# Kernel optimization log

Hardware: AMD Instinct MI355X
Metric: run time of the kernel (lower is better)

The kernel has to match this reference:

```python
import jax, jax.numpy as jnp
import numpy as np

B, S, H, NH, HD, F, L = 512, 32, 1024, 16, 64, 2048, 6
OBS_D, REF_D, ACT_D, MAX_REL = 256, 128, 32, 32
SCALE = 1.0 / np.sqrt(HD)
LN_EPS = 1e-5


def _ln(x, g, b):
    mu = x.mean(-1, keepdims=True)
    var = ((x - mu) ** 2).mean(-1, keepdims=True)
    return (x - mu) * jax.lax.rsqrt(var + LN_EPS) * g + b


def _mlp3(x, w0, b0, w1, b1, w2, b2):
    h = jax.nn.relu(x @ w0 + b0)
    h = jax.nn.relu(h @ w1 + b1)
    return h @ w2 + b2


def setup_inputs() -> dict:
    key = jax.random.key(0)
    ks = iter(jax.random.split(key, 64))

    def n(shape, scale=1.0):
        return (jax.random.normal(next(ks), shape, dtype=jnp.float32) * scale)

    W = 0.02  # weight scale (xavier-ish) to keep activations sane
    inp = {
        'obs': n((B, S, OBS_D)), 'ref': n((B, S, REF_D)),
        'obs_w0': n((OBS_D, 512), W), 'obs_b0': jnp.zeros((512,), jnp.float32),
        'obs_w1': n((512, 256), W), 'obs_b1': jnp.zeros((256,), jnp.float32),
        'obs_w2': n((256, H), W), 'obs_b2': jnp.zeros((H,), jnp.float32),
        'ref_w0': n((REF_D, 256), W), 'ref_b0': jnp.zeros((256,), jnp.float32),
        'ref_w1': n((256, 256), W), 'ref_b1': jnp.zeros((256,), jnp.float32),
        'ref_w2': n((256, H), W), 'ref_b2': jnp.zeros((H,), jnp.float32),
        'pos_emb': n((64, H), W),
        'Wq': n((L, H, H), W), 'Wk': n((L, H, H), W), 'Wv': n((L, H, H), W),
        'Wo': n((L, H, H), W), 'bo': jnp.zeros((L, H), jnp.float32),
        'rel_emb': n((L, 2 * MAX_REL + 1, HD), W),
        'ff_w1': n((L, H, F), W), 'ff_b1': jnp.zeros((L, F), jnp.float32),
        'ff_w2': n((L, F, H), W), 'ff_b2': jnp.zeros((L, H), jnp.float32),
        'ln1_g': jnp.ones((L, H), jnp.float32), 'ln1_b': jnp.zeros((L, H), jnp.float32),
        'ln2_g': jnp.ones((L, H), jnp.float32), 'ln2_b': jnp.zeros((L, H), jnp.float32),
        'act_w0': n((H, 256), W), 'act_b0': jnp.zeros((256,), jnp.float32),
        'act_w1': n((256, 128), W), 'act_b1': jnp.zeros((128,), jnp.float32),
        'act_w2': n((128, ACT_D), W), 'act_b2': jnp.zeros((ACT_D,), jnp.float32),
    }
    return inp


def _forward(obs, ref, obs_w0, obs_b0, obs_w1, obs_b1, obs_w2, obs_b2,
             ref_w0, ref_b0, ref_w1, ref_b1, ref_w2, ref_b2, pos_emb,
             Wq, Wk, Wv, Wo, bo, rel_emb, ff_w1, ff_b1, ff_w2, ff_b2,
             ln1_g, ln1_b, ln2_g, ln2_b,
             act_w0, act_b0, act_w1, act_b1, act_w2, act_b2):
    b, s, _ = obs.shape
    x = _mlp3(obs, obs_w0, obs_b0, obs_w1, obs_b1, obs_w2, obs_b2)
    x = x + _mlp3(ref, ref_w0, ref_b0, ref_w1, ref_b1, ref_w2, ref_b2)
    x = x + pos_emb[:s][None]  # learned positional encoding

    idx = jnp.arange(s)
    rel_idx = jnp.clip(idx[:, None] - idx[None, :], -MAX_REL, MAX_REL) + MAX_REL  # [S,S]

    def block(h, p):
        wq, wk, wv, wo, b_o, rel, w1, b1, w2, b2, g1, be1, g2, be2 = p
        xn = _ln(h, g1, be1)
        q = (xn @ wq).reshape(b, s, NH, HD)
        k = (xn @ wk).reshape(b, s, NH, HD)
        v = (xn @ wv).reshape(b, s, NH, HD)
        scores = jnp.einsum('bqhd,bkhd->bhqk', q, k) * SCALE
        rel_e = rel[rel_idx]  # [S,S,HD]
        scores = scores + jnp.einsum('bqhd,qkd->bhqk', q, rel_e)
        attn = jax.nn.softmax(scores, axis=-1)
        o = jnp.einsum('bhqk,bkhd->bqhd', attn, v).reshape(b, s, H)
        h = h + o @ wo + b_o
        xn2 = _ln(h, g2, be2)
        ff = jax.nn.gelu(xn2 @ w1 + b1, approximate=False) @ w2 + b2
        return h + ff, None

    x, _ = jax.lax.scan(block, x, (Wq, Wk, Wv, Wo, bo, rel_emb,
                                    ff_w1, ff_b1, ff_w2, ff_b2,
                                    ln1_g, ln1_b, ln2_g, ln2_b))
    return _mlp3(x[:, -1], act_w0, act_b0, act_w1, act_b1, act_w2, act_b2)


def reference(obs, ref, obs_w0, obs_b0, obs_w1, obs_b1, obs_w2, obs_b2,
              ref_w0, ref_b0, ref_w1, ref_b1, ref_w2, ref_b2, pos_emb,
              Wq, Wk, Wv, Wo, bo, rel_emb, ff_w1, ff_b1, ff_w2, ff_b2,
              ln1_g, ln1_b, ln2_g, ln2_b,
              act_w0, act_b0, act_w1, act_b1, act_w2, act_b2):
    return _forward(obs, ref, obs_w0, obs_b0, obs_w1, obs_b1, obs_w2, obs_b2,
                    ref_w0, ref_b0, ref_w1, ref_b1, ref_w2, ref_b2, pos_emb,
                    Wq, Wk, Wv, Wo, bo, rel_emb, ff_w1, ff_b1, ff_w2, ff_b2,
                    ln1_g, ln1_b, ln2_g, ln2_b,
                    act_w0, act_b0, act_w1, act_b1, act_w2, act_b2)
```

## Files before the change

### kernel.cpp

```cpp
#include <hip/hip_runtime.h>
#include <cstdint>
#include <cstddef>

typedef unsigned short u16;
typedef float f32x4 __attribute__((ext_vector_type(4)));
typedef short s16x8 __attribute__((ext_vector_type(8)));
typedef __bf16 bf16x8 __attribute__((ext_vector_type(8)));

#define DEVINL __device__ __forceinline__

DEVINL float bf2f(u16 u){ union{unsigned int i; float f;} c; c.i=((unsigned int)u)<<16; return c.f; }
DEVINL u16 f2bf(float f){ union{float f; unsigned int i;} c; c.f=f; unsigned int u=c.i;
                          u += 0x7FFF + ((u>>16)&1); return (u16)(u>>16); }

DEVINL f32x4 mfma16(bf16x8 a, bf16x8 b, f32x4 c){
  return __builtin_amdgcn_mfma_f32_16x16x32_bf16(a, b, c, 0, 0, 0);
}

typedef const __attribute__((address_space(1))) void* gas1p;
typedef __attribute__((address_space(3))) void* as3p;
DEVINL void async16(const void* g, void* l){
  __builtin_amdgcn_global_load_lds((gas1p)g, (as3p)l, 16, 0, 0);
}


__global__ void cvt_bf16(const float* __restrict__ in, u16* __restrict__ out, int n){
  int i = (blockIdx.x * 256 + threadIdx.x) * 4;
  if (i >= n) return;
  float4 v = *(const float4*)(in + i);
  short4 sv = make_short4((short)f2bf(v.x), (short)f2bf(v.y), (short)f2bf(v.z), (short)f2bf(v.w));
  *(short4*)(out + i) = sv;
}

__global__ __launch_bounds__(256) void trans_w(const float* __restrict__ W, u16* __restrict__ WT,
                                               int K, int N){
  __shared__ float t[32][33];
  const float* Wm = W  + (size_t)blockIdx.z * K * N;
  u16*         Tm = WT + (size_t)blockIdx.z * K * N;
  const int x = threadIdx.x, y = threadIdx.y;
  const int n0 = blockIdx.x * 32, k0 = blockIdx.y * 32;
#pragma unroll
  for (int j = 0; j < 32; j += 8)
    t[y + j][x] = Wm[(size_t)(k0 + y + j) * N + n0 + x];
  __syncthreads();
#pragma unroll
  for (int j = 0; j < 32; j += 8)
    Tm[(size_t)(n0 + y + j) * K + k0 + x] = f2bf(t[x][y + j]);
}


__global__ __launch_bounds__(256) void gemm128(
    const u16* __restrict__ A, const u16* __restrict__ BT,
    const float* __restrict__ bias, const float* __restrict__ resid,
    const float* __restrict__ pos, void* __restrict__ out,
    int M, int N, int K, int fuse)
{
  __shared__ u16 As[2][4096];
  __shared__ u16 Bs[2][4096];
  const int tid = threadIdx.x;
  const int bn = blockIdx.x, bm = blockIdx.y;
  const int lane = tid & 63, wid = tid >> 6;
  const int lr = lane & 15, lk = lane >> 4;
  const int wm = (wid >> 1) * 64, wn = (wid & 1) * 64;

  f32x4 acc[4][4] = {};

  const int r0 = tid >> 2;
  const int c0 = (tid & 3) * 8;
  const u16* Ab = A  + (size_t)(bm * 128 + r0) * K + c0;
  const u16* Bb = BT + (size_t)(bn * 128 + r0) * K + c0;
  const size_t rstep = (size_t)64 * K;
  const int nk = K >> 5;

  async16(Ab,         &As[0][tid * 8]);
  async16(Ab + rstep, &As[0][2048 + tid * 8]);
  async16(Bb,         &Bs[0][tid * 8]);
  async16(Bb + rstep, &Bs[0][2048 + tid * 8]);

  int cur = 0;
  for (int kt = 0; kt < nk; ++kt){
    __syncthreads();
    if (kt + 1 < nk){
      const u16* An = Ab + (size_t)(kt + 1) * 32;
      const u16* Bn = Bb + (size_t)(kt + 1) * 32;
      u16* Asn = &As[cur ^ 1][0];
      u16* Bsn = &Bs[cur ^ 1][0];
      async16(An,         Asn + tid * 8);
      async16(An + rstep, Asn + 2048 + tid * 8);
      async16(Bn,         Bsn + tid * 8);
      async16(Bn + rstep, Bsn + 2048 + tid * 8);
    }
    bf16x8 af[4], bfv[4];
#pragma unroll
    for (int i = 0; i < 4; ++i)
      af[i] = *(const bf16x8*)&As[cur][(wm + i * 16 + lr) * 32 + lk * 8];
#pragma unroll
    for (int j = 0; j < 4; ++j)
      bfv[j] = *(const bf16x8*)&Bs[cur][(wn + j * 16 + lr) * 32 + lk * 8];
#pragma unroll
    for (int i = 0; i < 4; ++i)
#pragma unroll
      for (int j = 0; j < 4; ++j)
        acc[i][j] = mfma16(af[i], bfv[j], acc[i][j]);
    cur ^= 1;
  }

  const int gm0 = bm * 128 + wm, gn0 = bn * 128 + wn;
  float* outf = (float*)out;
  u16*   outb = (u16*)out;
#pragma unroll
  for (int i = 0; i < 4; ++i){
#pragma unroll
    for (int j = 0; j < 4; ++j){
      const int col = gn0 + j * 16 + lr;
      const float bv = bias ? bias[col] : 0.f;
#pragma unroll
      for (int r = 0; r < 4; ++r){
        const int row = gm0 + i * 16 + lk * 4 + r;
        const size_t idx = (size_t)row * N + col;
        float v = acc[i][j][r] + bv;
        if (fuse == 1)      v = fmaxf(v, 0.f);
        else if (fuse == 2) v = 0.5f * v * (1.f + erff(v * 0.70710678118654752f));
        else if (fuse == 4) v += resid[idx];
        else if (fuse == 5) v += resid[idx] + pos[((row & 31) << 10) + col];
        if (fuse >= 3) outf[idx] = v;
        else           outb[idx] = f2bf(v);
      }
    }
  }
}


__global__ __launch_bounds__(256) void ln_k(
    const float* __restrict__ x, const float* __restrict__ g,
    const float* __restrict__ b, u16* __restrict__ out)
{
  const int row = blockIdx.x;
  const float* xr = x + (size_t)row * 1024;
  const int tid = threadIdx.x;
  float4 v = *(const float4*)(xr + tid * 4);
  float s  = v.x + v.y + v.z + v.w;
  float ss = v.x * v.x + v.y * v.y + v.z * v.z + v.w * v.w;
#pragma unroll
  for (int m = 1; m < 64; m <<= 1){ s += __shfl_xor(s, m, 64); ss += __shfl_xor(ss, m, 64); }
  __shared__ float red[8];
  if ((tid & 63) == 0){ red[tid >> 6] = s; red[4 + (tid >> 6)] = ss; }
  __syncthreads();
  s  = red[0] + red[1] + red[2] + red[3];
  ss = red[4] + red[5] + red[6] + red[7];
  const float mu = s * (1.f / 1024.f);
  const float rs = rsqrtf(ss * (1.f / 1024.f) - mu * mu + 1e-5f);
  float4 gg = *(const float4*)(g + tid * 4);
  float4 bb = *(const float4*)(b + tid * 4);
  short4 sv = make_short4((short)f2bf((v.x - mu) * rs * gg.x + bb.x),
                          (short)f2bf((v.y - mu) * rs * gg.y + bb.y),
                          (short)f2bf((v.z - mu) * rs * gg.z + bb.z),
                          (short)f2bf((v.w - mu) * rs * gg.w + bb.w));
  *(short4*)(out + (size_t)row * 1024 + tid * 4) = sv;
}


__global__ __launch_bounds__(256) void attn_k(
    const u16* __restrict__ Q, const u16* __restrict__ Kx,
    const u16* __restrict__ V, const u16* __restrict__ rel,
    u16* __restrict__ O)
{
  __shared__ char smem[65536];
  const int tid = threadIdx.x;
  const int wid = tid >> 6, lane = tid & 63;
  const int lr = lane & 15, lk = lane >> 4;
  char* sw = smem + wid * 16384;
  float* P = (float*)sw;
  u16*  AL = (u16*)(sw + 8704);
  u16*  VT = (u16*)(sw + 11264);

  const int pair = blockIdx.x * 4 + wid;
  const int b = pair >> 4, h = pair & 15;
  const size_t base = (size_t)b * 32768 + (size_t)h * 64;
  const u16* q  = Q  + base;
  const u16* kk = Kx + base;
  const u16* v  = V  + base;
  u16* o = O + base;

  s16x8 vv[4];
#pragma unroll
  for (int j = 0; j < 4; ++j){
    const int e = j * 64 + lane;
    const int ki = e >> 3, d0 = (e & 7) * 8;
    vv[j] = *(const s16x8*)(v + (size_t)ki * 1024 + d0);
  }

  bf16x8 qf[2][2], kf[2][2];
#pragma unroll
  for (int mf = 0; mf < 2; ++mf)
#pragma unroll
    for (int ks = 0; ks < 2; ++ks){
      qf[mf][ks] = *(const bf16x8*)(q  + (size_t)(mf * 16 + lr) * 1024 + ks * 32 + lk * 8);
      kf[mf][ks] = *(const bf16x8*)(kk + (size_t)(mf * 16 + lr) * 1024 + ks * 32 + lk * 8);
    }

  f32x4 sc[2][2] = {};
#pragma unroll
  for (int mf = 0; mf < 2; ++mf)
#pragma unroll
    for (int nf = 0; nf < 2; ++nf){
      sc[mf][nf] = mfma16(qf[mf][0], kf[nf][0], sc[mf][nf]);
      sc[mf][nf] = mfma16(qf[mf][1], kf[nf][1], sc[mf][nf]);
      sc[mf][nf] *= 0.125f;
    }

  f32x4 p[2][4] = {};
#pragma unroll
  for (int nf = 0; nf < 4; ++nf){
    bf16x8 rf0 = *(const bf16x8*)(rel + (nf * 16 + lr) * 64 + lk * 8);
    bf16x8 rf1 = *(const bf16x8*)(rel + (nf * 16 + lr) * 64 + 32 + lk * 8);
#pragma unroll
    for (int mf = 0; mf < 2; ++mf){
      p[mf][nf] = mfma16(qf[mf][0], rf0, p[mf][nf]);
      p[mf][nf] = mfma16(qf[mf][1], rf1, p[mf][nf]);
    }
  }

#pragma unroll
  for (int j = 0; j < 4; ++j){
    const int e = j * 64 + lane;
    const int ki = e >> 3, d0 = (e & 7) * 8;
#pragma unroll
    for (int i = 0; i < 8; ++i)
      VT[(d0 + i) * 40 + ki] = (u16)vv[j][i];
  }
#pragma unroll
  for (int mf = 0; mf < 2; ++mf)
#pragma unroll
    for (int nf = 0; nf < 4; ++nf)
#pragma unroll
      for (int r = 0; r < 4; ++r)
        P[(mf * 16 + lk * 4 + r) * 68 + nf * 16 + lr] = p[mf][nf][r];

  __syncthreads();

#pragma unroll
  for (int mf = 0; mf < 2; ++mf)
#pragma unroll
    for (int n2 = 0; n2 < 2; ++n2)
#pragma unroll
      for (int r = 0; r < 4; ++r){
        const int qr = mf * 16 + lk * 4 + r;
        const int kc = n2 * 16 + lr;
        sc[mf][n2][r] += P[qr * 68 + (qr - kc + 32)];
      }

#pragma unroll
  for (int mf = 0; mf < 2; ++mf)
#pragma unroll
    for (int r = 0; r < 4; ++r){
      float mx = fmaxf(sc[mf][0][r], sc[mf][1][r]);
#pragma unroll
      for (int m2 = 1; m2 < 16; m2 <<= 1) mx = fmaxf(mx, __shfl_xor(mx, m2, 64));
      const float e0 = __expf(sc[mf][0][r] - mx);
      const float e1 = __expf(sc[mf][1][r] - mx);
      float sm = e0 + e1;
#pragma unroll
      for (int m2 = 1; m2 < 16; m2 <<= 1) sm += __shfl_xor(sm, m2, 64);
      const float inv = 1.f / sm;
      sc[mf][0][r] = e0 * inv;
      sc[mf][1][r] = e1 * inv;
    }

#pragma unroll
  for (int mf = 0; mf < 2; ++mf)
#pragma unroll
    for (int n2 = 0; n2 < 2; ++n2)
#pragma unroll
      for (int r = 0; r < 4; ++r)
        AL[(mf * 16 + lk * 4 + r) * 40 + n2 * 16 + lr] = f2bf(sc[mf][n2][r]);

  __syncthreads();

  bf16x8 paf[2];
  paf[0] = *(const bf16x8*)&AL[(lr) * 40 + lk * 8];
  paf[1] = *(const bf16x8*)&AL[(16 + lr) * 40 + lk * 8];

  f32x4 of[2][4] = {};
#pragma unroll
  for (int nf = 0; nf < 4; ++nf){
    bf16x8 vf = *(const bf16x8*)&VT[(nf * 16 + lr) * 40 + lk * 8];
    of[0][nf] = mfma16(paf[0], vf, of[0][nf]);
    of[1][nf] = mfma16(paf[1], vf, of[1][nf]);
  }
#pragma unroll
  for (int mf = 0; mf < 2; ++mf)
#pragma unroll
    for (int nf = 0; nf < 4; ++nf)
#pragma unroll
      for (int r = 0; r < 4; ++r)
        o[(size_t)(mf * 16 + lk * 4 + r) * 1024 + nf * 16 + lr] = f2bf(of[mf][nf][r]);
}


__global__ void gather_last(const float* __restrict__ x, u16* __restrict__ out){
  const int i = blockIdx.x * 256 + threadIdx.x;
  const int b = i >> 10, c = i & 1023;
  out[i] = f2bf(x[((size_t)b * 32 + 31) * 1024 + c]);
}

__global__ void small_gemm(const u16* __restrict__ A, const u16* __restrict__ BT,
                           const float* __restrict__ bias, void* __restrict__ out,
                           int M, int N, int K, int fuse){
  const int idx = blockIdx.x * 256 + threadIdx.x;
  if (idx >= M * N) return;
  const int m = idx / N, n = idx - m * N;
  const u16* a  = A  + (size_t)m * K;
  const u16* bt = BT + (size_t)n * K;
  float acc = 0.f;
  for (int k = 0; k < K; k += 8){
    s16x8 av = *(const s16x8*)(a + k);
    s16x8 bv = *(const s16x8*)(bt + k);
#pragma unroll
    for (int i = 0; i < 8; ++i) acc += bf2f((u16)av[i]) * bf2f((u16)bv[i]);
  }
  float v = acc + bias[n];
  if (fuse == 1) v = fmaxf(v, 0.f);
  if (fuse == 3) ((float*)out)[idx] = v;
  else           ((u16*)out)[idx]   = f2bf(v);
}


extern "C" void kernel_launch(void* const* d_in, const int* in_sizes, int n_in,
                              void* d_out, int out_size, void* d_ws, size_t ws_size,
                              hipStream_t stream)
{
  (void)in_sizes; (void)n_in; (void)out_size;
  const float* obs    = (const float*)d_in[0];
  const float* refp   = (const float*)d_in[1];
  const float* obs_w0 = (const float*)d_in[2];
  const float* obs_b0 = (const float*)d_in[3];
  const float* obs_w1 = (const float*)d_in[4];
  const float* obs_b1 = (const float*)d_in[5];
  const float* obs_w2 = (const float*)d_in[6];
  const float* obs_b2 = (const float*)d_in[7];
  const float* ref_w0 = (const float*)d_in[8];
  const float* ref_b0 = (const float*)d_in[9];
  const float* ref_w1 = (const float*)d_in[10];
  const float* ref_b1 = (const float*)d_in[11];
  const float* ref_w2 = (const float*)d_in[12];
  const float* ref_b2 = (const float*)d_in[13];
  const float* pos    = (const float*)d_in[14];
  const float* Wq     = (const float*)d_in[15];
  const float* Wk     = (const float*)d_in[16];
  const float* Wv     = (const float*)d_in[17];
  const float* Wo     = (const float*)d_in[18];
  const float* bo     = (const float*)d_in[19];
  const float* rel    = (const float*)d_in[20];
  const float* ff_w1  = (const float*)d_in[21];
  const float* ff_b1  = (const float*)d_in[22];
  const float* ff_w2  = (const float*)d_in[23];
  const float* ff_b2  = (const float*)d_in[24];
  const float* ln1g   = (const float*)d_in[25];
  const float* ln1b   = (const float*)d_in[26];
  const float* ln2g   = (const float*)d_in[27];
  const float* ln2b   = (const float*)d_in[28];
  const float* act_w0 = (const float*)d_in[29];
  const float* act_b0 = (const float*)d_in[30];
  const float* act_w1 = (const float*)d_in[31];
  const float* act_b1 = (const float*)d_in[32];
  const float* act_w2 = (const float*)d_in[33];
  const float* act_b2 = (const float*)d_in[34];
  float* outp = (float*)d_out;

  char* wsp = (char*)d_ws; size_t off = 0;
  auto alloc = [&](size_t bytes)->char*{ char* p = wsp + off;
                                         off = (off + bytes + 255) & ~(size_t)255; return p; };

  u16* wt_obs0 = (u16*)alloc((size_t)512 * 256 * 2);
  u16* wt_obs1 = (u16*)alloc((size_t)256 * 512 * 2);
  u16* wt_obs2 = (u16*)alloc((size_t)1024 * 256 * 2);
  u16* wt_ref0 = (u16*)alloc((size_t)256 * 128 * 2);
  u16* wt_ref1 = (u16*)alloc((size_t)256 * 256 * 2);
  u16* wt_ref2 = (u16*)alloc((size_t)1024 * 256 * 2);
  u16* wt_a0   = (u16*)alloc((size_t)256 * 1024 * 2);
  u16* wt_a1   = (u16*)alloc((size_t)128 * 256 * 2);
  u16* wt_a2   = (u16*)alloc((size_t)32 * 128 * 2);
  u16* rel_bf  = (u16*)alloc((size_t)6 * 65 * 64 * 2);
  u16* wt_lq   = (u16*)alloc((size_t)1024 * 1024 * 2);
  u16* wt_lk   = (u16*)alloc((size_t)1024 * 1024 * 2);
  u16* wt_lv   = (u16*)alloc((size_t)1024 * 1024 * 2);
  u16* wt_lo   = (u16*)alloc((size_t)1024 * 1024 * 2);
  u16* wt_lf1  = (u16*)alloc((size_t)2048 * 1024 * 2);
  u16* wt_lf2  = (u16*)alloc((size_t)2048 * 1024 * 2);
  float* x     = (float*)alloc((size_t)16384 * 1024 * 4);
  u16* xn      = (u16*)alloc((size_t)16384 * 1024 * 2);
  u16* qb      = (u16*)alloc((size_t)16384 * 1024 * 2);
  u16* kb      = (u16*)alloc((size_t)16384 * 1024 * 2);
  u16* vb      = (u16*)alloc((size_t)16384 * 1024 * 2);

  if (off > ws_size) return;

  u16* obs_bf = qb;
  u16* h1     = kb;
  u16* h2     = vb;
  u16* ref_bf = xn;
  u16* ob     = xn;
  u16* ffb    = qb;
  u16* xlast  = qb;
  u16* a1b    = kb;
  u16* a2b    = vb;

  auto CV = [&](const float* src, u16* dst, int n){
    cvt_bf16<<<dim3((n / 4 + 255) / 256), dim3(256), 0, stream>>>(src, dst, n);
  };
  auto TR = [&](const float* W, u16* WT, int Kd, int Nd, int nz){
    trans_w<<<dim3(Nd / 32, Kd / 32, nz), dim3(32, 8), 0, stream>>>(W, WT, Kd, Nd);
  };
  auto GM = [&](const u16* A, const u16* BT, const float* bias, const float* resid,
                const float* posb, void* op, int Md, int Nd, int Kd, int fuse){
    gemm128<<<dim3(Nd / 128, Md / 128), dim3(256), 0, stream>>>(A, BT, bias, resid, posb, op, Md, Nd, Kd, fuse);
  };

  CV(rel, rel_bf, 6 * 65 * 64);
  TR(obs_w0, wt_obs0, 256, 512, 1);
  TR(obs_w1, wt_obs1, 512, 256, 1);
  TR(obs_w2, wt_obs2, 256, 1024, 1);
  TR(ref_w0, wt_ref0, 128, 256, 1);
  TR(ref_w1, wt_ref1, 256, 256, 1);
  TR(ref_w2, wt_ref2, 256, 1024, 1);
  TR(act_w0, wt_a0, 1024, 256, 1);
  TR(act_w1, wt_a1, 256, 128, 1);
  TR(act_w2, wt_a2, 128, 32, 1);

  const int M = 16384;
  CV(obs, obs_bf, 16384 * 256);
  GM(obs_bf, wt_obs0, obs_b0, nullptr, nullptr, h1, M, 512, 256, 1);
  GM(h1,     wt_obs1, obs_b1, nullptr, nullptr, h2, M, 256, 512, 1);
  GM(h2,     wt_obs2, obs_b2, nullptr, nullptr, x,  M, 1024, 256, 3);
  CV(refp, ref_bf, 16384 * 128);
  GM(ref_bf, wt_ref0, ref_b0, nullptr, nullptr, h2, M, 256, 128, 1);
  GM(h2,     wt_ref1, ref_b1, nullptr, nullptr, h1, M, 256, 256, 1);
  GM(h1,     wt_ref2, ref_b2, x, pos,           x,  M, 1024, 256, 5);

  for (int l = 0; l < 6; ++l){
    TR(Wq + (size_t)l * 1048576, wt_lq, 1024, 1024, 1);
    TR(Wk + (size_t)l * 1048576, wt_lk, 1024, 1024, 1);
    TR(Wv + (size_t)l * 1048576, wt_lv, 1024, 1024, 1);
    TR(Wo + (size_t)l * 1048576, wt_lo, 1024, 1024, 1);
    TR(ff_w1 + (size_t)l * 2097152, wt_lf1, 1024, 2048, 1);
    TR(ff_w2 + (size_t)l * 2097152, wt_lf2, 2048, 1024, 1);

    ln_k<<<dim3(16384), dim3(256), 0, stream>>>(x, ln1g + l * 1024, ln1b + l * 1024, xn);
    GM(xn, wt_lq, nullptr, nullptr, nullptr, qb, M, 1024, 1024, 0);
    GM(xn, wt_lk, nullptr, nullptr, nullptr, kb, M, 1024, 1024, 0);
    GM(xn, wt_lv, nullptr, nullptr, nullptr, vb, M, 1024, 1024, 0);
    attn_k<<<dim3(2048), dim3(256), 0, stream>>>(qb, kb, vb, rel_bf + (size_t)l * 4160, ob);
    GM(ob, wt_lo, bo + l * 1024, x, nullptr, x, M, 1024, 1024, 4);
    ln_k<<<dim3(16384), dim3(256), 0, stream>>>(x, ln2g + l * 1024, ln2b + l * 1024, xn);
    GM(xn,  wt_lf1, ff_b1 + l * 2048, nullptr, nullptr, ffb, M, 2048, 1024, 2);
    GM(ffb, wt_lf2, ff_b2 + l * 1024, x, nullptr, x, M, 1024, 2048, 4);
  }

  gather_last<<<dim3(2048), dim3(256), 0, stream>>>(x, xlast);
  small_gemm<<<dim3(512 * 256 / 256), dim3(256), 0, stream>>>(xlast, wt_a0, act_b0, a1b, 512, 256, 1024, 1);
  small_gemm<<<dim3(512 * 128 / 256), dim3(256), 0, stream>>>(a1b, wt_a1, act_b1, a2b, 512, 128, 256, 1);
  small_gemm<<<dim3(512 * 32 / 256),  dim3(256), 0, stream>>>(a2b, wt_a2, act_b2, outp, 512, 32, 128, 3);
}
```

Measured before the change: 4.510 ms.

## Fuse Q/K/V projections into one GEMM and add XCD-aware block swizzle

Concatenates the transposed Wq, Wk and Wv into one 3072x1024 weight and runs a single GEMM writing an interleaved QKV buffer. The attention kernel now reads Q, K and V with a 3072 row stride. It also remaps GEMM workgroup IDs so that consecutive tiles land on the same XCD, which should improve L2 reuse. The fused GEMM reads the normalized activations once instead of three times and cuts launches, but attention loads become more strided.

```diff
diff --git a/kernel.cpp b/kernel.cpp
--- a/kernel.cpp
+++ b/kernel.cpp
@@ -58,7 +58,15 @@
   __shared__ u16 As[2][4096];
   __shared__ u16 Bs[2][4096];
   const int tid = threadIdx.x;
-  const int bn = blockIdx.x, bm = blockIdx.y;
+
+  const int nbn = gridDim.x;
+  const int nwg = gridDim.x * gridDim.y;
+  const int lid = blockIdx.y * nbn + blockIdx.x;
+  const int q8 = nwg >> 3, r8 = nwg & 7;
+  const int xcd = lid & 7, posi = lid >> 3;
+  const int swz = (xcd < r8 ? xcd * (q8 + 1) : r8 * (q8 + 1) + (xcd - r8) * q8) + posi;
+  const int bm = swz / nbn, bn = swz - bm * nbn;
+
   const int lane = tid & 63, wid = tid >> 6;
   const int lr = lane & 15, lk = lane >> 4;
   const int wm = (wid >> 1) * 64, wn = (wid & 1) * 64;
@@ -161,8 +169,7 @@
 
 
 __global__ __launch_bounds__(256) void attn_k(
-    const u16* __restrict__ Q, const u16* __restrict__ Kx,
-    const u16* __restrict__ V, const u16* __restrict__ rel,
+    const u16* __restrict__ QKV, const u16* __restrict__ rel,
     u16* __restrict__ O)
 {
   __shared__ char smem[65536];
@@ -176,18 +183,17 @@
 
   const int pair = blockIdx.x * 4 + wid;
   const int b = pair >> 4, h = pair & 15;
-  const size_t base = (size_t)b * 32768 + (size_t)h * 64;
-  const u16* q  = Q  + base;
-  const u16* kk = Kx + base;
-  const u16* v  = V  + base;
-  u16* o = O + base;
+  const u16* q  = QKV + (size_t)b * 32 * 3072 + (size_t)h * 64;
+  const u16* kk = q + 1024;
+  const u16* v  = q + 2048;
+  u16* o = O + (size_t)b * 32768 + (size_t)h * 64;
 
   s16x8 vv[4];
 #pragma unroll
   for (int j = 0; j < 4; ++j){
     const int e = j * 64 + lane;
     const int ki = e >> 3, d0 = (e & 7) * 8;
-    vv[j] = *(const s16x8*)(v + (size_t)ki * 1024 + d0);
+    vv[j] = *(const s16x8*)(v + (size_t)ki * 3072 + d0);
   }
 
   bf16x8 qf[2][2], kf[2][2];
@@ -195,8 +201,8 @@
   for (int mf = 0; mf < 2; ++mf)
 #pragma unroll
     for (int ks = 0; ks < 2; ++ks){
-      qf[mf][ks] = *(const bf16x8*)(q  + (size_t)(mf * 16 + lr) * 1024 + ks * 32 + lk * 8);
-      kf[mf][ks] = *(const bf16x8*)(kk + (size_t)(mf * 16 + lr) * 1024 + ks * 32 + lk * 8);
+      qf[mf][ks] = *(const bf16x8*)(q  + (size_t)(mf * 16 + lr) * 3072 + ks * 32 + lk * 8);
+      kf[mf][ks] = *(const bf16x8*)(kk + (size_t)(mf * 16 + lr) * 3072 + ks * 32 + lk * 8);
     }
 
   f32x4 sc[2][2] = {};
@@ -382,29 +388,25 @@
   u16* wt_a1   = (u16*)alloc((size_t)128 * 256 * 2);
   u16* wt_a2   = (u16*)alloc((size_t)32 * 128 * 2);
   u16* rel_bf  = (u16*)alloc((size_t)6 * 65 * 64 * 2);
-  u16* wt_lq   = (u16*)alloc((size_t)1024 * 1024 * 2);
-  u16* wt_lk   = (u16*)alloc((size_t)1024 * 1024 * 2);
-  u16* wt_lv   = (u16*)alloc((size_t)1024 * 1024 * 2);
+  u16* wt_qkv  = (u16*)alloc((size_t)3072 * 1024 * 2);
   u16* wt_lo   = (u16*)alloc((size_t)1024 * 1024 * 2);
   u16* wt_lf1  = (u16*)alloc((size_t)2048 * 1024 * 2);
   u16* wt_lf2  = (u16*)alloc((size_t)2048 * 1024 * 2);
   float* x     = (float*)alloc((size_t)16384 * 1024 * 4);
   u16* xn      = (u16*)alloc((size_t)16384 * 1024 * 2);
-  u16* qb      = (u16*)alloc((size_t)16384 * 1024 * 2);
-  u16* kb      = (u16*)alloc((size_t)16384 * 1024 * 2);
-  u16* vb      = (u16*)alloc((size_t)16384 * 1024 * 2);
+  u16* qkv     = (u16*)alloc((size_t)16384 * 3072 * 2);
 
   if (off > ws_size) return;
 
-  u16* obs_bf = qb;
-  u16* h1     = kb;
-  u16* h2     = vb;
+  u16* obs_bf = qkv;
+  u16* h1     = qkv + (size_t)16384 * 256;
+  u16* h2     = qkv + (size_t)16384 * 768;
   u16* ref_bf = xn;
   u16* ob     = xn;
-  u16* ffb    = qb;
-  u16* xlast  = qb;
-  u16* a1b    = kb;
-  u16* a2b    = vb;
+  u16* ffb    = qkv;
+  u16* xlast  = qkv;
+  u16* a1b    = qkv + (size_t)16384 * 256;
+  u16* a2b    = qkv + (size_t)16384 * 512;
 
   auto CV = [&](const float* src, u16* dst, int n){
     cvt_bf16<<<dim3((n / 4 + 255) / 256), dim3(256), 0, stream>>>(src, dst, n);
@@ -439,18 +441,16 @@
   GM(h1,     wt_ref2, ref_b2, x, pos,           x,  M, 1024, 256, 5);
 
   for (int l = 0; l < 6; ++l){
-    TR(Wq + (size_t)l * 1048576, wt_lq, 1024, 1024, 1);
-    TR(Wk + (size_t)l * 1048576, wt_lk, 1024, 1024, 1);
-    TR(Wv + (size_t)l * 1048576, wt_lv, 1024, 1024, 1);
+    TR(Wq + (size_t)l * 1048576, wt_qkv,                        1024, 1024, 1);
+    TR(Wk + (size_t)l * 1048576, wt_qkv + (size_t)1024 * 1024,  1024, 1024, 1);
+    TR(Wv + (size_t)l * 1048576, wt_qkv + (size_t)2048 * 1024,  1024, 1024, 1);
     TR(Wo + (size_t)l * 1048576, wt_lo, 1024, 1024, 1);
     TR(ff_w1 + (size_t)l * 2097152, wt_lf1, 1024, 2048, 1);
     TR(ff_w2 + (size_t)l * 2097152, wt_lf2, 2048, 1024, 1);
 
     ln_k<<<dim3(16384), dim3(256), 0, stream>>>(x, ln1g + l * 1024, ln1b + l * 1024, xn);
-    GM(xn, wt_lq, nullptr, nullptr, nullptr, qb, M, 1024, 1024, 0);
-    GM(xn, wt_lk, nullptr, nullptr, nullptr, kb, M, 1024, 1024, 0);
-    GM(xn, wt_lv, nullptr, nullptr, nullptr, vb, M, 1024, 1024, 0);
-    attn_k<<<dim3(2048), dim3(256), 0, stream>>>(qb, kb, vb, rel_bf + (size_t)l * 4160, ob);
+    GM(xn, wt_qkv, nullptr, nullptr, nullptr, qkv, M, 3072, 1024, 0);
+    attn_k<<<dim3(2048), dim3(256), 0, stream>>>(qkv, rel_bf + (size_t)l * 4160, ob);
     GM(ob, wt_lo, bo + l * 1024, x, nullptr, x, M, 1024, 1024, 4);
     ln_k<<<dim3(16384), dim3(256), 0, stream>>>(x, ln2g + l * 1024, ln2b + l * 1024, xn);
     GM(xn,  wt_lf1, ff_b1 + l * 2048, nullptr, nullptr, ffb, M, 2048, 1024, 2);
```

Measured after the change: 3.981 ms. 11.7% less time.
